# Kernel tuning notes

Hardware: AMD Instinct MI355X
Metric: run time of the kernel (lower is better)

The kernel has to match this reference:

```python
import jax, jax.numpy as jnp
import numpy as np
from fractions import Fraction
from math import factorial

LMAX1 = 3
LMAX2 = 3
LMAX_OUT = 3
DIM1 = (LMAX1 + 1) ** 2  # 16
DIM2 = (LMAX2 + 1) ** 2  # 16
N = 2_000_000


def _su2_cg(j1, m1, j2, m2, j3, m3):
    # exact SU(2) Clebsch-Gordan coefficient <j1 m1 j2 m2 | j3 m3>
    if m3 != m1 + m2:
        return 0.0
    vmin = int(max(-j1 + j2 + m3, -j1 + m1, 0))
    vmax = int(min(j2 + j3 + m1, j3 - j1 + j2, j3 + m3))
    f = factorial
    C = (2 * j3 + 1) * Fraction(
        f(j3 + j1 - j2) * f(j3 - j1 + j2) * f(j1 + j2 - j3) * f(j3 + m3) * f(j3 - m3),
        f(j1 + j2 + j3 + 1) * f(j1 - m1) * f(j1 + m1) * f(j2 - m2) * f(j2 + m2),
    )
    S = Fraction(0)
    for v in range(vmin, vmax + 1):
        S += (-1) ** (v + j2 + m2) * Fraction(
            f(j2 + j3 + m1 - v) * f(j1 - m1 + v),
            f(v) * f(j3 - j1 + j2 - v) * f(j3 + m3 - v) * f(v + j1 - j2 - m3),
        )
    return float(C) ** 0.5 * float(S)


def _su2_cg_matrix(j1, j2, j3):
    mat = np.zeros((2 * j1 + 1, 2 * j2 + 1, 2 * j3 + 1))
    if abs(j1 - j2) <= j3 <= j1 + j2:
        for m1 in range(-j1, j1 + 1):
            for m2 in range(-j2, j2 + 1):
                m3 = m1 + m2
                if abs(m3) <= j3:
                    mat[j1 + m1, j2 + m2, j3 + m3] = _su2_cg(j1, m1, j2, m2, j3, m3)
    return mat


def _change_basis_real_to_complex(l):
    q = np.zeros((2 * l + 1, 2 * l + 1), dtype=complex)
    for m in range(-l, 0):
        q[l + m, l + abs(m)] = 1.0 / np.sqrt(2)
        q[l + m, l - abs(m)] = -1j / np.sqrt(2)
    q[l, l] = 1.0
    for m in range(1, l + 1):
        q[l + m, l + abs(m)] = (-1) ** m / np.sqrt(2)
        q[l + m, l - abs(m)] = 1j * (-1) ** m / np.sqrt(2)
    return (-1j) ** l * q


def CG_SO3(l1, l2, l3):
    # real-spherical-harmonics Wigner 3j / CG tensor, shape (2l1+1, 2l2+1, 2l3+1)
    Q1 = _change_basis_real_to_complex(l1)
    Q2 = _change_basis_real_to_complex(l2)
    Q3 = _change_basis_real_to_complex(l3)
    C = _su2_cg_matrix(l1, l2, l3).astype(complex)
    C = np.einsum('ij,kl,mn,ikn->jlm', Q1, Q2, np.conj(Q3.T), C)
    return np.real(C)


def _build_w3j():
    irreps_1 = [(l, (-1) ** l) for l in range(LMAX1 + 1)]
    irreps_2 = [(l, (-1) ** l) for l in range(LMAX2 + 1)]
    irreps_out = [(l, (-1) ** l) for l in range(LMAX_OUT + 1)]
    s1 = np.cumsum([0] + [2 * l + 1 for l, _ in irreps_1])
    s2 = np.cumsum([0] + [2 * l + 1 for l, _ in irreps_2])
    so = np.cumsum([0] + [2 * l + 1 for l, _ in irreps_out])
    w3js = []
    for iout, (lout, pout) in enumerate(irreps_out):
        for i1, (l1, p1) in enumerate(irreps_1):
            for i2, (l2, p2) in enumerate(irreps_2):
                if pout != p1 * p2:
                    continue
                if lout > l1 + l2 or lout < abs(l1 - l2):
                    continue
                w3j = CG_SO3(l1, l2, lout)
                full = np.zeros((DIM1, DIM2, DIM1))
                scale = (2 * lout + 1) ** 0.5
                full[s1[i1]:s1[i1 + 1], s2[i2]:s2[i2 + 1], so[iout]:so[iout + 1]] = w3j * scale
                w3js.append(full)
    return np.stack(w3js).astype(np.float32)  # (npath=23, 16, 16, 16)


_W3J = _build_w3j()
NPATH = _W3J.shape[0]


def setup_inputs() -> dict:
    key = jax.random.key(0)
    k1, k2, k3 = jax.random.split(key, 3)
    x1 = jax.random.normal(k1, (N, DIM1), dtype=jnp.float32)
    x2 = jax.random.normal(k2, (N, DIM2), dtype=jnp.float32)
    # flax param init: jax.nn.initializers.normal() -> stddev 0.01
    weights = 0.01 * jax.random.normal(k3, (NPATH,), dtype=jnp.float32)
    return {"x1": x1, "x2": x2, "weights": weights}


def reference(x1, x2, weights):
    w3j = jnp.asarray(_W3J)  # (p, a, b, c) constant CG tensor
    ww3j = jnp.einsum('p,pabc->abc', weights, w3j)  # (16, 16, 16)
    return jnp.einsum('...a,...b,abc->...c', x1, x2, ww3j)  # (N, 16)
```

## Files before the change

kernel.cpp:

```cpp
#include <hip/hip_runtime.h>


struct Tables {
  int npaths;
  int pl1[32], pl2[32], plo[32];
  int nent;
  int pstart[33];
  unsigned char ea[512], eb[512], ec[512];
};

constexpr Tables build_tables() {
  Tables t{};
  for (int lo = 0; lo <= 3; ++lo)
    for (int l1 = 0; l1 <= 3; ++l1)
      for (int l2 = 0; l2 <= 3; ++l2) {
        if (((l1 + l2 + lo) & 1) != 0) continue;
        int lmin = l1 > l2 ? l1 - l2 : l2 - l1;
        if (lo > l1 + l2 || lo < lmin) continue;
        int p = t.npaths;
        t.pl1[p] = l1; t.pl2[p] = l2; t.plo[p] = lo;
        t.pstart[p] = t.nent;
        int o1 = l1 * l1, o2 = l2 * l2, oo = lo * lo;
        for (int m1 = -l1; m1 <= l1; ++m1)
          for (int m2 = -l2; m2 <= l2; ++m2) {
            int cand[2]; int nc = 0;
            if (m1 == 0) cand[nc++] = m2;
            else if (m2 == 0) cand[nc++] = m1;
            else {
              int u = m1 < 0 ? -m1 : m1, v = m2 < 0 ? -m2 : m2;
              int d = u > v ? u - v : v - u;
              if ((m1 > 0) == (m2 > 0)) {
                cand[nc++] = u + v; cand[nc++] = d;
              } else {
                cand[nc++] = -(u + v);
                if (d) cand[nc++] = -d;
              }
            }
            for (int q = 0; q < nc; ++q) {
              int m3 = cand[q];
              int am3 = m3 < 0 ? -m3 : m3;
              if (am3 <= lo) {
                t.ea[t.nent] = (unsigned char)(o1 + l1 + m1);
                t.eb[t.nent] = (unsigned char)(o2 + l2 + m2);
                t.ec[t.nent] = (unsigned char)(oo + lo + m3);
                ++t.nent;
              }
            }
          }
        ++t.npaths;
        t.pstart[t.npaths] = t.nent;
      }
  return t;
}

constexpr Tables TBL = build_tables();
constexpr int NENT = TBL.nent;
constexpr int NCREG = (NENT + 63) / 64;

__device__ __constant__ double FACT[11] = {
    1., 1., 2., 6., 24., 120., 720., 5040., 40320., 362880., 3628800.};

struct cplx { double re, im; };

__device__ inline double su2_cg(int j1, int m1, int j2, int m2, int j3, int m3) {
  if (m3 != m1 + m2) return 0.0;
  int vmin = -j1 + j2 + m3;
  if (-j1 + m1 > vmin) vmin = -j1 + m1;
  if (0 > vmin) vmin = 0;
  int vmax = j2 + j3 + m1;
  if (j3 - j1 + j2 < vmax) vmax = j3 - j1 + j2;
  if (j3 + m3 < vmax) vmax = j3 + m3;
  double C = (2.0 * j3 + 1.0) *
             (FACT[j3 + j1 - j2] * FACT[j3 - j1 + j2] * FACT[j1 + j2 - j3] *
              FACT[j3 + m3] * FACT[j3 - m3]) /
             (FACT[j1 + j2 + j3 + 1] * FACT[j1 - m1] * FACT[j1 + m1] *
              FACT[j2 - m2] * FACT[j2 + m2]);
  double S = 0.0;
  for (int v = vmin; v <= vmax; ++v) {
    double t = (FACT[j2 + j3 + m1 - v] * FACT[j1 - m1 + v]) /
               (FACT[v] * FACT[j3 - j1 + j2 - v] * FACT[j3 + m3 - v] *
                FACT[v + j1 - j2 - m3]);
    S += (((v + j2 + m2) & 1) ? -1.0 : 1.0) * t;
  }
  return sqrt(C) * S;
}

__device__ inline cplx Qmat(int l, int r, int c) {
  int m = r - l, mc = c - l;
  const double is2 = 0.70710678118654752440;
  double re = 0.0, im = 0.0;
  if (m < 0) {
    if (mc == -m) re = is2;
    else if (mc == m) im = -is2;
  } else if (m == 0) {
    if (mc == 0) re = 1.0;
  } else {
    double s = (m & 1) ? -is2 : is2;
    if (mc == m) re = s;
    else if (mc == -m) im = s;
  }
  cplx out;
  switch (l & 3) {
    case 0: out.re = re;  out.im = im;  break;
    case 1: out.re = im;  out.im = -re; break;
    case 2: out.re = -re; out.im = -im; break;
    default: out.re = -im; out.im = re; break;
  }
  return out;
}

__global__ void cg_setup_kernel(const float* __restrict__ weights,
                                float* __restrict__ wwc) {
  const int p = blockIdx.x;
  const int l1 = TBL.pl1[p], l2 = TBL.pl2[p], lo = TBL.plo[p];
  const int n1 = 2 * l1 + 1, n2 = 2 * l2 + 1, n3 = 2 * lo + 1;
  const int tot = n1 * n2 * n3;
  const int tid = (int)threadIdx.x;
  const int bd = (int)blockDim.x;

  __shared__ double Cs[343];
  __shared__ double Vr[343], Vi[343];
  __shared__ double Ur[343], Ui[343];
  __shared__ double Rr[343];

  for (int idx = tid; idx < tot; idx += bd) {
    int i = idx / (n2 * n3), r = idx % (n2 * n3);
    int k = r / n3, nn = r % n3;
    Cs[idx] = su2_cg(l1, i - l1, l2, k - l2, lo, nn - lo);
  }
  __syncthreads();

  for (int idx = tid; idx < tot; idx += bd) {
    int i = idx / (n2 * n3), r = idx % (n2 * n3);
    int k = r / n3, m = r % n3;
    double vr = 0.0, vi = 0.0;
    for (int nn = 0; nn < n3; ++nn) {
      double c = Cs[(i * n2 + k) * n3 + nn];
      cplx q = Qmat(lo, nn, m);
      vr += c * q.re;
      vi -= c * q.im;
    }
    Vr[idx] = vr; Vi[idx] = vi;
  }
  __syncthreads();

  for (int idx = tid; idx < tot; idx += bd) {
    int i = idx / (n2 * n3), r = idx % (n2 * n3);
    int l = r / n3, m = r % n3;
    double ur = 0.0, ui = 0.0;
    for (int k = 0; k < n2; ++k) {
      cplx q = Qmat(l2, k, l);
      double vr = Vr[(i * n2 + k) * n3 + m];
      double vi = Vi[(i * n2 + k) * n3 + m];
      ur += q.re * vr - q.im * vi;
      ui += q.re * vi + q.im * vr;
    }
    Ur[idx] = ur; Ui[idx] = ui;
  }
  __syncthreads();

  for (int idx = tid; idx < tot; idx += bd) {
    int j = idx / (n2 * n3), r = idx % (n2 * n3);
    int l = r / n3, m = r % n3;
    double rr = 0.0;
    for (int i = 0; i < n1; ++i) {
      cplx q = Qmat(l1, i, j);
      rr += q.re * Ur[(i * n2 + l) * n3 + m] - q.im * Ui[(i * n2 + l) * n3 + m];
    }
    Rr[idx] = rr;
  }
  __syncthreads();

  const double ws = (double)weights[p] * sqrt(2.0 * lo + 1.0);
  const int o1 = l1 * l1, o2 = l2 * l2, oo = lo * lo;
  for (int e = TBL.pstart[p] + tid; e < TBL.pstart[p + 1]; e += bd) {
    int i = (int)TBL.ea[e] - o1;
    int j = (int)TBL.eb[e] - o2;
    int k = (int)TBL.ec[e] - oo;
    wwc[e] = (float)(ws * Rr[(i * n2 + j) * n3 + k]);
  }
}

__global__ __launch_bounds__(256) void tp_kernel(const float* __restrict__ x1,
                                                 const float* __restrict__ x2,
                                                 const float* __restrict__ wwc,
                                                 float* __restrict__ out,
                                                 int n) {
  const int lane = (int)threadIdx.x & 63;

  float creg[NCREG];
#pragma unroll
  for (int k = 0; k < NCREG; ++k) creg[k] = wwc[k * 64 + lane];

  const int row = (int)blockIdx.x * 256 + (int)threadIdx.x;
  if (row >= n) return;

  const float4* X1 = reinterpret_cast<const float4*>(x1) + (size_t)row * 4;
  const float4* X2 = reinterpret_cast<const float4*>(x2) + (size_t)row * 4;

  float a[16], b[16];
#pragma unroll
  for (int q = 0; q < 4; ++q) {
    float4 t = X1[q];
    a[4 * q + 0] = t.x; a[4 * q + 1] = t.y; a[4 * q + 2] = t.z; a[4 * q + 3] = t.w;
    float4 u = X2[q];
    b[4 * q + 0] = u.x; b[4 * q + 1] = u.y; b[4 * q + 2] = u.z; b[4 * q + 3] = u.w;
  }

  float acc[16];
#pragma unroll
  for (int c = 0; c < 16; ++c) acc[c] = 0.0f;

#pragma unroll
  for (int e = 0; e < NENT; ++e) {
    int wbits = __builtin_amdgcn_readlane(__float_as_int(creg[e >> 6]), e & 63);
    float w = __int_as_float(wbits);
    acc[TBL.ec[e]] = fmaf(w, a[TBL.ea[e]] * b[TBL.eb[e]], acc[TBL.ec[e]]);
  }

  float4* O = reinterpret_cast<float4*>(out) + (size_t)row * 4;
#pragma unroll
  for (int q = 0; q < 4; ++q) {
    O[q] = make_float4(acc[4 * q + 0], acc[4 * q + 1], acc[4 * q + 2],
                       acc[4 * q + 3]);
  }
}

extern "C" void kernel_launch(void* const* d_in, const int* in_sizes, int n_in,
                              void* d_out, int out_size, void* d_ws,
                              size_t ws_size, hipStream_t stream) {
  const float* x1 = (const float*)d_in[0];
  const float* x2 = (const float*)d_in[1];
  const float* w  = (const float*)d_in[2];
  float* out = (float*)d_out;
  float* wwc = (float*)d_ws;

  const int n = in_sizes[0] / 16;

  cg_setup_kernel<<<dim3(TBL.npaths), dim3(256), 0, stream>>>(w, wwc);

  const int grid = (n + 255) / 256;
  tp_kernel<<<dim3(grid), dim3(256), 0, stream>>>(x1, x2, wwc, out, n);
}
```

Measured before the change: 308.7 us.

## Reorder CG entries by (a,b) pair, use scalar weight loads and nontemporal stores

Builds a compile-time schedule that sorts the sparse CG entries by (a,b) input pair, so each product a*b is computed once and shared across the outputs that use it. The first write to each accumulator becomes a plain multiply, which removes the zero initialisation. Weights are now read straight from global memory with uniform indices, so the compiler can use scalar loads instead of a per-lane register table plus readlane. Output uses nontemporal vector stores to avoid polluting the cache. The setup kernel now scans the whole schedule for every path to fill the reordered weight array, which adds a little setup work.

Result: slower. 388.8 us (+25.9%).

```diff
diff --git a/kernel.cpp b/kernel.cpp
--- a/kernel.cpp
+++ b/kernel.cpp
@@ -1,12 +1,14 @@
 #include <hip/hip_runtime.h>
 
+
+typedef float v4f __attribute__((ext_vector_type(4)));
 
 struct Tables {
   int npaths;
   int pl1[32], pl2[32], plo[32];
   int nent;
   int pstart[33];
-  unsigned char ea[512], eb[512], ec[512];
+  unsigned char ea[512], eb[512], ec[512], ep[512];
 };
 
 constexpr Tables build_tables() {
@@ -23,7 +25,7 @@
         int o1 = l1 * l1, o2 = l2 * l2, oo = lo * lo;
         for (int m1 = -l1; m1 <= l1; ++m1)
           for (int m2 = -l2; m2 <= l2; ++m2) {
-            int cand[2]; int nc = 0;
+            int cand[2] = {0, 0}; int nc = 0;
             if (m1 == 0) cand[nc++] = m2;
             else if (m2 == 0) cand[nc++] = m1;
             else {
@@ -43,6 +45,7 @@
                 t.ea[t.nent] = (unsigned char)(o1 + l1 + m1);
                 t.eb[t.nent] = (unsigned char)(o2 + l2 + m2);
                 t.ec[t.nent] = (unsigned char)(oo + lo + m3);
+                t.ep[t.nent] = (unsigned char)p;
                 ++t.nent;
               }
             }
@@ -54,8 +57,43 @@
 }
 
 constexpr Tables TBL = build_tables();
-constexpr int NENT = TBL.nent;
-constexpr int NCREG = (NENT + 63) / 64;
+
+struct Sched {
+  int nent;
+  unsigned char sa[512], sb[512], sc[512], sp[512];
+  bool newpair[512];
+  bool firstc[512];
+};
+
+constexpr Sched build_sched() {
+  Sched s{};
+  int pos = 0;
+  bool seen[16] = {};
+  for (int a = 0; a < 16; ++a)
+    for (int b = 0; b < 16; ++b) {
+      bool first_of_pair = true;
+      for (int e = 0; e < TBL.nent; ++e) {
+        if ((int)TBL.ea[e] == a && (int)TBL.eb[e] == b) {
+          s.sa[pos] = (unsigned char)a;
+          s.sb[pos] = (unsigned char)b;
+          s.sc[pos] = TBL.ec[e];
+          s.sp[pos] = TBL.ep[e];
+          s.newpair[pos] = first_of_pair;
+          s.firstc[pos] = !seen[TBL.ec[e]];
+          seen[TBL.ec[e]] = true;
+          first_of_pair = false;
+          ++pos;
+        }
+      }
+    }
+  s.nent = pos;
+  return s;
+}
+
+constexpr Sched SCH = build_sched();
+constexpr int NENT = SCH.nent;
+static_assert(SCH.nent == TBL.nent, "schedule must cover all entries");
+static_assert(SCH.nent <= 512, "table overflow");
 
 __device__ __constant__ double FACT[11] = {
     1., 1., 2., 6., 24., 120., 720., 5040., 40320., 362880., 3628800.};
@@ -171,13 +209,14 @@
   }
   __syncthreads();
 
-  const double ws = (double)weights[p] * sqrt(2.0 * lo + 1.0);
+  const double wsc = (double)weights[p] * sqrt(2.0 * lo + 1.0);
   const int o1 = l1 * l1, o2 = l2 * l2, oo = lo * lo;
-  for (int e = TBL.pstart[p] + tid; e < TBL.pstart[p + 1]; e += bd) {
-    int i = (int)TBL.ea[e] - o1;
-    int j = (int)TBL.eb[e] - o2;
-    int k = (int)TBL.ec[e] - oo;
-    wwc[e] = (float)(ws * Rr[(i * n2 + j) * n3 + k]);
+  for (int s = tid; s < NENT; s += bd) {
+    if ((int)SCH.sp[s] != p) continue;
+    int i = (int)SCH.sa[s] - o1;
+    int j = (int)SCH.sb[s] - o2;
+    int k = (int)SCH.sc[s] - oo;
+    wwc[s] = (float)(wsc * Rr[(i * n2 + j) * n3 + k]);
   }
 }
 
@@ -186,12 +225,6 @@
                                                  const float* __restrict__ wwc,
                                                  float* __restrict__ out,
                                                  int n) {
-  const int lane = (int)threadIdx.x & 63;
-
-  float creg[NCREG];
-#pragma unroll
-  for (int k = 0; k < NCREG; ++k) creg[k] = wwc[k * 64 + lane];
-
   const int row = (int)blockIdx.x * 256 + (int)threadIdx.x;
   if (row >= n) return;
 
@@ -208,21 +241,23 @@
   }
 
   float acc[16];
-#pragma unroll
-  for (int c = 0; c < 16; ++c) acc[c] = 0.0f;
+  float t = 0.0f;
 
 #pragma unroll
   for (int e = 0; e < NENT; ++e) {
-    int wbits = __builtin_amdgcn_readlane(__float_as_int(creg[e >> 6]), e & 63);
-    float w = __int_as_float(wbits);
-    acc[TBL.ec[e]] = fmaf(w, a[TBL.ea[e]] * b[TBL.eb[e]], acc[TBL.ec[e]]);
-  }
-
-  float4* O = reinterpret_cast<float4*>(out) + (size_t)row * 4;
+    if (SCH.newpair[e]) t = a[SCH.sa[e]] * b[SCH.sb[e]];
+    const float w = wwc[e];
+    if (SCH.firstc[e]) acc[SCH.sc[e]] = w * t;
+    else               acc[SCH.sc[e]] = fmaf(w, t, acc[SCH.sc[e]]);
+  }
+
+  v4f* O = reinterpret_cast<v4f*>(out) + (size_t)row * 4;
 #pragma unroll
   for (int q = 0; q < 4; ++q) {
-    O[q] = make_float4(acc[4 * q + 0], acc[4 * q + 1], acc[4 * q + 2],
-                       acc[4 * q + 3]);
+    v4f o;
+    o.x = acc[4 * q + 0]; o.y = acc[4 * q + 1];
+    o.z = acc[4 * q + 2]; o.w = acc[4 * q + 3];
+    __builtin_nontemporal_store(o, &O[q]);
   }
 }
 
```
